# Kernel tuning notes

Hardware: AMD Instinct MI355X
Metric: run time of the kernel (lower is better)

## Reference

```python
import jax, jax.numpy as jnp
import numpy as np

R, A, E, K, NREL = 2048, 16384, 131072, 48, 7
RADIUS = 10.0


def setup_inputs():
    key = jax.random.key(0)
    ks = jax.random.split(key, 20)
    f = jax.random.normal
    return {
        "node_feature": f(ks[0], (R, 21), jnp.float32),
        "all_atom_pos": f(ks[1], (A, 3), jnp.float32) * 8.0,
        "atom_name": jax.random.randint(ks[2], (A,), 0, 38),
        "ca_idx": jax.random.randint(ks[3], (R,), 0, A),
        "edge_src": jax.random.randint(ks[4], (E,), 0, R),
        "edge_dst": jax.random.randint(ks[5], (E,), 0, R),
        "edge_rel": jax.random.randint(ks[6], (E,), 0, NREL),
        # parameters (atom-type embedding table, residue-type linear, AEP point MLP,
        # relational graph conv, env2structures MLP with BN)
        "emb_atom": f(ks[7], (39, 64), jnp.float32) * 0.02,
        "Wres": f(ks[8], (21, 64), jnp.float32) * 0.1,
        "bres": jnp.zeros((64,), jnp.float32),
        "Wxyz": f(ks[9], (3, 64), jnp.float32) * 0.1,
        "W1": f(ks[10], (64, 128), jnp.float32) * 0.1,
        "b1": jnp.zeros((128,), jnp.float32),
        "W2": f(ks[11], (128, 256), jnp.float32) * 0.08,
        "b2": jnp.zeros((256,), jnp.float32),
        "Wconv": f(ks[12], (NREL * 64, 512), jnp.float32) * 0.05,
        "bconv": jnp.zeros((512,), jnp.float32),
        "Wself": f(ks[13], (64, 512), jnp.float32) * 0.1,
        "We1": f(ks[14], (512 + 256, 512), jnp.float32) * 0.05,
        "be1": jnp.zeros((512,), jnp.float32),
        "gamma1": jnp.ones((512,), jnp.float32),
        "beta1": jnp.zeros((512,), jnp.float32),
        "We2": f(ks[15], (512, 512), jnp.float32) * 0.05,
        "be2": jnp.zeros((512,), jnp.float32),
    }


def reference(node_feature, all_atom_pos, atom_name, ca_idx, edge_src, edge_dst, edge_rel,
              emb_atom, Wres, bres, Wxyz, W1, b1, W2, b2,
              Wconv, bconv, Wself, We1, be1, gamma1, beta1, We2, be2):
    # residue-type embedding (nn.Linear(21, 64))
    res_feat = node_feature @ Wres + bres                      # [R,64]
    # ball query: each CA gathers all-atom neighbors within RADIUS (fixed K, masked)
    ca = all_atom_pos[ca_idx]                                   # [R,3]
    diff = ca[:, None, :] - all_atom_pos[None, :, :]            # [R,A,3]
    d = jnp.sqrt(jnp.sum(diff * diff, axis=-1) + 1e-12)         # [R,A]
    dm = jnp.where(d < RADIUS, d, jnp.inf)
    negd, nbr = jax.lax.top_k(-dm, K)                           # K nearest in ball
    mask = (-negd) < RADIUS                                     # [R,K]
    maskf = mask.astype(res_feat.dtype)[..., None]
    delta = (all_atom_pos[nbr] - ca[:, None, :]) * maskf        # relative coords [R,K,3]
    # padded atom-type embedding (padding contributes zeros, like padding_idx=38)
    pts = (emb_atom[atom_name[nbr]] + delta @ Wxyz) * maskf     # [R,K,64]
    # AEP point MLP + masked max-pool -> environment feature
    h = jax.nn.relu(pts @ W1 + b1)                              # [R,K,128]
    env = jnp.max(jnp.where(mask[..., None], h, -1e9), axis=1)  # [R,128]
    env = jax.nn.relu(env @ W2 + b2)                            # [R,256]
    # relational graph conv: per-relation scatter-sum over destination nodes
    seg = edge_dst * NREL + edge_rel
    agg = jax.ops.segment_sum(res_feat[edge_src], seg, num_segments=R * NREL)
    agg = agg.reshape(R, NREL * res_feat.shape[1])              # [R, 7*64]
    hres = jax.nn.relu(agg @ Wconv + bconv + res_feat @ Wself)  # [R,512]
    # env2structures MLP (Linear -> BatchNorm1d(train stats) -> ReLU -> Linear)
    z = jnp.concatenate([hres, env], axis=-1) @ We1 + be1       # [R,512]
    z = (z - z.mean(0)) * jax.lax.rsqrt(z.var(0) + 1e-5) * gamma1 + beta1
    return jax.nn.relu(z) @ We2 + be2                           # [R,512]
```

## Files before the change

### kernel.cpp

```cpp
#include <hip/hip_runtime.h>
#include <math.h>

#define R_ 2048
#define A_ 16384
#define E_ 131072
#define K_ 48
#define NREL_ 7

typedef __attribute__((ext_vector_type(8))) short bfrag8;
typedef __attribute__((ext_vector_type(4))) float f32x4v;

__device__ __forceinline__ unsigned short bf16rne(float f) {
    unsigned u = __builtin_bit_cast(unsigned, f);
    u += 0x7FFFu + ((u >> 16) & 1u);
    return (unsigned short)(u >> 16);
}

__device__ __forceinline__ float dist2(float x, float y, float z,
                                       float cx, float cy, float cz) {
    float dx = x - cx, dy = y - cy, dz = z - cz;
    return fmaf(dx, dx, fmaf(dy, dy, dz * dz));
}

__global__ __launch_bounds__(256) void k_prep(
    const float* __restrict__ Wconv, const float* __restrict__ Wself,
    const float* __restrict__ We1, const float* __restrict__ We2,
    const float* __restrict__ W1,
    const float* __restrict__ node, const float* __restrict__ Wres,
    const float* __restrict__ bres,
    unsigned short* __restrict__ Bt1, unsigned short* __restrict__ Bt2,
    unsigned short* __restrict__ Bt3, unsigned short* __restrict__ W1t,
    float* __restrict__ resfeat, float* __restrict__ bufA,
    float* __restrict__ stats)
{
    int id = blockIdx.x * 256 + threadIdx.x;
    if (id < 262144) {
        int k = id & 511, n = id >> 9;
        float v = (k < 448) ? Wconv[k * 512 + n] : Wself[(k - 448) * 512 + n];
        Bt1[n * 512 + k] = bf16rne(v);
    } else if (id < 655360) {
        int rel = id - 262144;
        int k = rel % 768, n = rel / 768;
        Bt2[n * 768 + k] = bf16rne(We1[k * 512 + n]);
    } else if (id < 917504) {
        int rel = id - 655360;
        int k = rel & 511, n = rel >> 9;
        Bt3[n * 512 + k] = bf16rne(We2[k * 512 + n]);
    } else if (id < 925696) {
        int rel = id - 917504;
        int k = rel & 63, n = rel >> 6;
        W1t[n * 64 + k] = bf16rne(W1[k * 128 + n]);
    } else if (id < 1056768) {
        int rel = id - 925696;
        int r = rel >> 6, c = rel & 63;
        float s = bres[c];
#pragma unroll
        for (int i = 0; i < 21; ++i) s += node[r * 21 + i] * Wres[i * 64 + c];
        resfeat[r * 64 + c] = s;
        bufA[(size_t)r * 512 + 448 + c] = s;
    } else if (id < 1974272) {
        int rel = id - 1056768;
        int r = rel / 448, c = rel % 448;
        bufA[(size_t)r * 512 + c] = 0.f;
    } else if (id < 1975296) {
        stats[id - 1974272] = 0.f;
    }
}

__global__ __launch_bounds__(256) void k_edges(
    const int* __restrict__ esrc, const int* __restrict__ edst,
    const int* __restrict__ erel, const float* __restrict__ resfeat,
    float* __restrict__ bufA)
{
    int idx = blockIdx.x * 256 + threadIdx.x;
    int e = idx >> 6, c = idx & 63;
    int d = edst[e], rel = erel[e], s = esrc[e];
    atomicAdd(&bufA[(size_t)d * 512 + rel * 64 + c], resfeat[s * 64 + c]);
}

__global__ __launch_bounds__(256) void k_ball_env(
    const float* __restrict__ pos, const int* __restrict__ ca_idx,
    const int* __restrict__ atom_name,
    const float* __restrict__ emb, const float* __restrict__ Wxyz,
    const unsigned short* __restrict__ W1t,
    const float* __restrict__ b1,
    const float* __restrict__ W2, const float* __restrict__ b2,
    float* __restrict__ outZ1)
{
    __shared__ __align__(16) char SB[33792];
    __shared__ int s_list[64];
    __shared__ unsigned s_cnt, s_ccnt;
    __shared__ int sB, sNeed, sB2, sNeed2, sTotal;

    unsigned* binsw = (unsigned*)SB;
    unsigned* hist  = (unsigned*)(SB + 16384);
    unsigned* hist2 = (unsigned*)(SB + 17408);
    int*      sc    = (int*)(SB + 18432);
    float*    candd = (float*)(SB + 19456);
    int*      candi = (int*)(SB + 19968);

    float*          pts    = (float*)SB;
    unsigned short* W1s    = (unsigned short*)(SB + 13056);
    float*          sWxyz  = (float*)(SB + 31488);
    float*          s_dv   = (float*)(SB + 32256);
    float*          env128 = (float*)(SB + 32832);
    int*            s_an   = (int*)(SB + 33344);
    int*            s_aa   = (int*)(SB + 33536);

    int tid = threadIdx.x;
    int r = blockIdx.x;
    int ca = ca_idx[r];
    float cx = pos[ca * 3 + 0], cy = pos[ca * 3 + 1], cz = pos[ca * 3 + 2];

    hist[tid] = 0u;
    if (tid == 0) { s_cnt = 0u; s_ccnt = 0u; }
    __syncthreads();

    for (int it = 0; it < 16; ++it) {
        int a0 = it * 1024 + tid * 4;
        const float4* p = (const float4*)(pos + (size_t)a0 * 3);
        float4 p0 = p[0], p1 = p[1], p2 = p[2];
        float xs[4] = { p0.x, p0.w, p1.z, p2.y };
        float ys[4] = { p0.y, p1.x, p1.w, p2.z };
        float zs[4] = { p0.z, p1.y, p2.x, p2.w };
        unsigned pack = 0;
#pragma unroll
        for (int q = 0; q < 4; ++q) {
            float d2 = dist2(xs[q], ys[q], zs[q], cx, cy, cz);
            int b = 255;
            if (d2 < 100.0f) {
                b = (int)(d2 * 2.56f); if (b > 254) b = 254;
                atomicAdd(&hist[b], 1u);
            }
            pack |= (unsigned)b << (q * 8);
        }
        binsw[it * 256 + tid] = pack;
    }
    __syncthreads();

    sc[tid] = (int)hist[tid];
    __syncthreads();
    for (int s = 1; s < 256; s <<= 1) {
        int v = (tid >= s) ? sc[tid - s] : 0;
        __syncthreads();
        sc[tid] += v;
        __syncthreads();
    }
    if (tid == 0) sTotal = sc[255];
    if (sc[tid] >= K_ && (tid == 0 || sc[tid - 1] < K_)) {
        sB = tid;
        sNeed = K_ - (sc[tid] - (int)hist[tid]);
    }
    __syncthreads();

    int mode = (sTotal <= K_) ? 0 : (((int)hist[sB] > 128) ? 2 : 1);

    if (mode <= 1) {
        int B = (mode == 0) ? 255 : sB;
        for (int it = 0; it < 16; ++it) {
            unsigned pack = binsw[it * 256 + tid];
            int a0 = it * 1024 + tid * 4;
#pragma unroll
            for (int q = 0; q < 4; ++q) {
                int b = (pack >> (q * 8)) & 255;
                if (b < B) { unsigned pp = atomicAdd(&s_cnt, 1u); s_list[pp] = a0 + q; }
                else if (b == B && mode == 1) {
                    unsigned c = atomicAdd(&s_ccnt, 1u);
                    if (c < 128u) candi[c] = a0 + q;
                }
            }
        }
    } else {
        int B = sB;
        float lo2 = B * 0.390625f;
        hist2[tid] = 0u;
        __syncthreads();
        for (int it = 0; it < 16; ++it) {
            unsigned pack = binsw[it * 256 + tid];
            int a0 = it * 1024 + tid * 4;
#pragma unroll
            for (int q = 0; q < 4; ++q) {
                if (((pack >> (q * 8)) & 255) == (unsigned)B) {
                    int a = a0 + q;
                    float d2 = dist2(pos[a * 3], pos[a * 3 + 1], pos[a * 3 + 2], cx, cy, cz);
                    int k2 = (int)((d2 - lo2) * 655.36f);
                    if (k2 < 0) k2 = 0; if (k2 > 255) k2 = 255;
                    atomicAdd(&hist2[k2], 1u);
                }
            }
        }
        __syncthreads();
        sc[tid] = (int)hist2[tid];
        __syncthreads();
        for (int s = 1; s < 256; s <<= 1) {
            int v = (tid >= s) ? sc[tid - s] : 0;
            __syncthreads();
            sc[tid] += v;
            __syncthreads();
        }
        if (sc[tid] >= sNeed && (tid == 0 || sc[tid - 1] < sNeed)) {
            sB2 = tid;
            sNeed2 = sNeed - (sc[tid] - (int)hist2[tid]);
        }
        __syncthreads();
        int B2 = sB2;
        for (int it = 0; it < 16; ++it) {
            unsigned pack = binsw[it * 256 + tid];
            int a0 = it * 1024 + tid * 4;
#pragma unroll
            for (int q = 0; q < 4; ++q) {
                int b = (pack >> (q * 8)) & 255;
                if (b < B) { unsigned pp = atomicAdd(&s_cnt, 1u); s_list[pp] = a0 + q; }
                else if (b == B) {
                    int a = a0 + q;
                    float d2 = dist2(pos[a * 3], pos[a * 3 + 1], pos[a * 3 + 2], cx, cy, cz);
                    int k2 = (int)((d2 - lo2) * 655.36f);
                    if (k2 < 0) k2 = 0; if (k2 > 255) k2 = 255;
                    if (k2 < B2) { unsigned pp = atomicAdd(&s_cnt, 1u); s_list[pp] = a; }
                    else if (k2 == B2) {
                        unsigned c = atomicAdd(&s_ccnt, 1u);
                        if (c < 128u) candi[c] = a;
                    }
                }
            }
        }
    }
    __syncthreads();

    int needN = (mode == 0) ? 0 : ((mode == 1) ? sNeed : sNeed2);
    unsigned C = s_ccnt; if (C > 128u) C = 128u;
    if (tid < (int)C) {
        int a = candi[tid];
        float d2 = dist2(pos[a * 3], pos[a * 3 + 1], pos[a * 3 + 2], cx, cy, cz);
        candd[tid] = sqrtf(d2 + 1e-12f);
    }
    __syncthreads();
    if (tid < (int)C) {
        float di = candd[tid]; int ii = candi[tid];
        int rank = 0;
        for (unsigned j = 0; j < C; ++j) {
            float dj = candd[j]; int ij = candi[j];
            if (dj < di || (dj == di && ij < ii)) ++rank;
        }
        if (rank < needN) { unsigned pp = atomicAdd(&s_cnt, 1u); s_list[pp] = ii; }
    }
    __syncthreads();

    unsigned nb = s_cnt;

    for (int c = tid; c < 1024; c += 256)
        *(uint4*)((char*)W1s + (c >> 3) * 144 + (c & 7) * 16) = ((const uint4*)W1t)[c];
    if (tid < 192) sWxyz[tid] = Wxyz[tid];
    if (tid < K_) {
        int a = (tid < (int)nb) ? s_list[tid] : -1;
        s_aa[tid] = a;
        if (a >= 0) {
            s_dv[tid * 3 + 0] = pos[a * 3 + 0] - cx;
            s_dv[tid * 3 + 1] = pos[a * 3 + 1] - cy;
            s_dv[tid * 3 + 2] = pos[a * 3 + 2] - cz;
            s_an[tid] = atom_name[a];
        } else {
            s_dv[tid * 3 + 0] = 0.f; s_dv[tid * 3 + 1] = 0.f; s_dv[tid * 3 + 2] = 0.f;
            s_an[tid] = 0;
        }
    }
    __syncthreads();

    for (int idx = tid; idx < K_ * 64; idx += 256) {
        int row = idx >> 6, k = idx & 63;
        int a = s_aa[row];
        float v = 0.f;
        if (a >= 0) {
            v = emb[s_an[row] * 64 + k]
              + s_dv[row * 3 + 0] * sWxyz[k] + s_dv[row * 3 + 1] * sWxyz[64 + k]
              + s_dv[row * 3 + 2] * sWxyz[128 + k];
        }
        pts[row * 68 + k] = v;
    }
    __syncthreads();

    int w = tid >> 6, l = tid & 63;
    int fr = l & 15, fo = l >> 4;
    f32x4v acc[3][2];
#pragma unroll
    for (int m = 0; m < 3; ++m)
#pragma unroll
        for (int n = 0; n < 2; ++n) acc[m][n] = (f32x4v){0.f, 0.f, 0.f, 0.f};

#pragma unroll
    for (int ks = 0; ks < 2; ++ks) {
        bfrag8 af[3], bf[2];
#pragma unroll
        for (int m = 0; m < 3; ++m) {
            int row = 16 * m + fr;
            const char* base = (const char*)pts + row * 272 + ks * 128 + fo * 32;
            float4 v0 = *(const float4*)base;
            float4 v1 = *(const float4*)(base + 16);
            bfrag8 t;
            t[0] = (short)bf16rne(v0.x); t[1] = (short)bf16rne(v0.y);
            t[2] = (short)bf16rne(v0.z); t[3] = (short)bf16rne(v0.w);
            t[4] = (short)bf16rne(v1.x); t[5] = (short)bf16rne(v1.y);
            t[6] = (short)bf16rne(v1.z); t[7] = (short)bf16rne(v1.w);
            af[m] = t;
        }
#pragma unroll
        for (int n = 0; n < 2; ++n) {
            int wrow = (2 * w + n) * 16 + fr;
            bf[n] = *(const bfrag8*)((const char*)W1s + wrow * 144 + ks * 64 + fo * 16);
        }
#pragma unroll
        for (int m = 0; m < 3; ++m)
#pragma unroll
            for (int n = 0; n < 2; ++n)
                acc[m][n] = __builtin_amdgcn_mfma_f32_16x16x32_bf16(af[m], bf[n], acc[m][n], 0, 0, 0);
    }

#pragma unroll
    for (int n = 0; n < 2; ++n) {
        int col = 32 * w + n * 16 + fr;
        float bv = b1[col];
        float m = -1e30f;
#pragma unroll
        for (int mt = 0; mt < 3; ++mt) {
#pragma unroll
            for (int i = 0; i < 4; ++i) {
                int row = 16 * mt + fo * 4 + i;
                if (s_aa[row] >= 0) m = fmaxf(m, fmaxf(acc[mt][n][i] + bv, 0.f));
            }
        }
        m = fmaxf(m, __shfl_xor(m, 16));
        m = fmaxf(m, __shfl_xor(m, 32));
        if (fo == 0 && (l & 48) == 0) env128[col] = m;
    }
    __syncthreads();

    {
        float s = b2[tid];
        for (int i = 0; i < 128; ++i) s += env128[i] * W2[i * 256 + tid];
        outZ1[(size_t)r * 768 + 512 + tid] = fmaxf(s, 0.f);
    }
}

template<bool RELU_OUT, bool BN_A, bool STATS>
__global__ __launch_bounds__(256) void k_mgemm(
    const float* __restrict__ A, int lda, int K,
    const unsigned short* __restrict__ Bt,
    const float* __restrict__ bias,
    const float* __restrict__ stats, const float* __restrict__ gamma,
    const float* __restrict__ beta,
    float* __restrict__ C, int ldc, float* __restrict__ statsOut)
{
    __shared__ __align__(16) unsigned short As[64 * 32];
    __shared__ __align__(16) unsigned short Bs[64 * 32];
    __shared__ float bnsc[BN_A ? 512 : 1];
    __shared__ float bnsh[BN_A ? 512 : 1];

    int tid = threadIdx.x;
    int m0 = blockIdx.y * 64, n0 = blockIdx.x * 64;

    if (BN_A) {
        for (int i = tid; i < 512; i += 256) {
            float mean = stats[i] * (1.0f / 2048.0f);
            float var = stats[512 + i] * (1.0f / 2048.0f) - mean * mean;
            float inv = 1.0f / sqrtf(var + 1e-5f);
            float scv = gamma[i] * inv;
            bnsc[i] = scv;
            bnsh[i] = beta[i] - mean * scv;
        }
        __syncthreads();
    }

    int w = tid >> 6, l = tid & 63;
    int wm = w >> 1, wn = w & 1;

    int ar = tid >> 2, aslot = tid & 3, acg = aslot * 8;
    int abyte = ar * 64 + ((aslot ^ ((ar >> 1) & 3)) << 4);
    int bn_ = tid >> 2, bslot = tid & 3;
    int bbyte = bn_ * 64 + ((bslot ^ ((bn_ >> 1) & 3)) << 4);

    int fr = l & 15, fo = l >> 4;
    int ar0 = 32 * wm + fr, ar1 = ar0 + 16;
    int af0 = ar0 * 64 + ((fo ^ ((ar0 >> 1) & 3)) << 4);
    int af1 = ar1 * 64 + ((fo ^ ((ar1 >> 1) & 3)) << 4);
    int bc0 = 32 * wn + fr, bc1 = bc0 + 16;
    int bf0o = bc0 * 64 + ((fo ^ ((bc0 >> 1) & 3)) << 4);
    int bf1o = bc1 * 64 + ((fo ^ ((bc1 >> 1) & 3)) << 4);

    f32x4v acc00 = {0.f,0.f,0.f,0.f}, acc01 = {0.f,0.f,0.f,0.f};
    f32x4v acc10 = {0.f,0.f,0.f,0.f}, acc11 = {0.f,0.f,0.f,0.f};

    for (int k0 = 0; k0 < K; k0 += 32) {
        const float* ap = A + (size_t)(m0 + ar) * lda + k0 + acg;
        float4 v0 = *(const float4*)ap;
        float4 v1 = *(const float4*)(ap + 4);
        uint4 bv = *(const uint4*)(Bt + (size_t)(n0 + bn_) * K + k0 + bslot * 8);
        if (BN_A) {
            int kb = k0 + acg;
            v0.x = fmaxf(v0.x * bnsc[kb + 0] + bnsh[kb + 0], 0.f);
            v0.y = fmaxf(v0.y * bnsc[kb + 1] + bnsh[kb + 1], 0.f);
            v0.z = fmaxf(v0.z * bnsc[kb + 2] + bnsh[kb + 2], 0.f);
            v0.w = fmaxf(v0.w * bnsc[kb + 3] + bnsh[kb + 3], 0.f);
            v1.x = fmaxf(v1.x * bnsc[kb + 4] + bnsh[kb + 4], 0.f);
            v1.y = fmaxf(v1.y * bnsc[kb + 5] + bnsh[kb + 5], 0.f);
            v1.z = fmaxf(v1.z * bnsc[kb + 6] + bnsh[kb + 6], 0.f);
            v1.w = fmaxf(v1.w * bnsc[kb + 7] + bnsh[kb + 7], 0.f);
        }
        uint4 aw;
        aw.x = (unsigned)bf16rne(v0.x) | ((unsigned)bf16rne(v0.y) << 16);
        aw.y = (unsigned)bf16rne(v0.z) | ((unsigned)bf16rne(v0.w) << 16);
        aw.z = (unsigned)bf16rne(v1.x) | ((unsigned)bf16rne(v1.y) << 16);
        aw.w = (unsigned)bf16rne(v1.z) | ((unsigned)bf16rne(v1.w) << 16);
        __syncthreads();
        *(uint4*)((char*)As + abyte) = aw;
        *(uint4*)((char*)Bs + bbyte) = bv;
        __syncthreads();

        bfrag8 a0 = *(const bfrag8*)((const char*)As + af0);
        bfrag8 a1 = *(const bfrag8*)((const char*)As + af1);
        bfrag8 b0 = *(const bfrag8*)((const char*)Bs + bf0o);
        bfrag8 b1f = *(const bfrag8*)((const char*)Bs + bf1o);
        acc00 = __builtin_amdgcn_mfma_f32_16x16x32_bf16(a0, b0, acc00, 0, 0, 0);
        acc01 = __builtin_amdgcn_mfma_f32_16x16x32_bf16(a0, b1f, acc01, 0, 0, 0);
        acc10 = __builtin_amdgcn_mfma_f32_16x16x32_bf16(a1, b0, acc10, 0, 0, 0);
        acc11 = __builtin_amdgcn_mfma_f32_16x16x32_bf16(a1, b1f, acc11, 0, 0, 0);
    }

    int col0 = n0 + 32 * wn + fr;
    int row0 = m0 + 32 * wm + fo * 4;
    float bb0 = bias[col0], bb1 = bias[col0 + 16];
    float s0 = 0.f, q0 = 0.f, s1 = 0.f, q1 = 0.f;
#pragma unroll
    for (int i = 0; i < 4; ++i) {
        float u00 = acc00[i] + bb0, u01 = acc01[i] + bb1;
        float u10 = acc10[i] + bb0, u11 = acc11[i] + bb1;
        if (RELU_OUT) {
            u00 = fmaxf(u00, 0.f); u01 = fmaxf(u01, 0.f);
            u10 = fmaxf(u10, 0.f); u11 = fmaxf(u11, 0.f);
        }
        if (STATS) {
            s0 += u00 + u10; q0 += u00 * u00 + u10 * u10;
            s1 += u01 + u11; q1 += u01 * u01 + u11 * u11;
        }
        C[(size_t)(row0 + i) * ldc + col0] = u00;
        C[(size_t)(row0 + i) * ldc + col0 + 16] = u01;
        C[(size_t)(row0 + 16 + i) * ldc + col0] = u10;
        C[(size_t)(row0 + 16 + i) * ldc + col0 + 16] = u11;
    }
    if (STATS) {
        s0 += __shfl_xor(s0, 16); s0 += __shfl_xor(s0, 32);
        q0 += __shfl_xor(q0, 16); q0 += __shfl_xor(q0, 32);
        s1 += __shfl_xor(s1, 16); s1 += __shfl_xor(s1, 32);
        q1 += __shfl_xor(q1, 16); q1 += __shfl_xor(q1, 32);
        if (fo == 0) {
            atomicAdd(&statsOut[col0], s0);
            atomicAdd(&statsOut[512 + col0], q0);
            atomicAdd(&statsOut[col0 + 16], s1);
            atomicAdd(&statsOut[512 + col0 + 16], q1);
        }
    }
}

extern "C" void kernel_launch(void* const* d_in, const int* in_sizes, int n_in,
                              void* d_out, int out_size, void* d_ws, size_t ws_size,
                              hipStream_t stream)
{
    const float* node   = (const float*)d_in[0];
    const float* pos    = (const float*)d_in[1];
    const int*   aname  = (const int*)d_in[2];
    const int*   caidx  = (const int*)d_in[3];
    const int*   esrc   = (const int*)d_in[4];
    const int*   edst   = (const int*)d_in[5];
    const int*   erel   = (const int*)d_in[6];
    const float* emb    = (const float*)d_in[7];
    const float* Wres   = (const float*)d_in[8];
    const float* bres   = (const float*)d_in[9];
    const float* Wxyz   = (const float*)d_in[10];
    const float* W1     = (const float*)d_in[11];
    const float* b1     = (const float*)d_in[12];
    const float* W2     = (const float*)d_in[13];
    const float* b2     = (const float*)d_in[14];
    const float* Wconv  = (const float*)d_in[15];
    const float* bconv  = (const float*)d_in[16];
    const float* Wself  = (const float*)d_in[17];
    const float* We1    = (const float*)d_in[18];
    const float* be1    = (const float*)d_in[19];
    const float* gamma1 = (const float*)d_in[20];
    const float* beta1  = (const float*)d_in[21];
    const float* We2    = (const float*)d_in[22];
    const float* be2    = (const float*)d_in[23];
    float* out = (float*)d_out;

    char* ws = (char*)d_ws;
    float* resfeat = (float*)(ws + 0);
    float* bufA    = (float*)(ws + 524288);
    float* bufZ1   = (float*)(ws + 4718592);
    float* bufZ2   = (float*)(ws + 11010048);
    float* stats   = (float*)(ws + 15204352);
    unsigned short* Bt1 = (unsigned short*)(ws + 15208448);
    unsigned short* Bt2 = (unsigned short*)(ws + 15732736);
    unsigned short* Bt3 = (unsigned short*)(ws + 16519168);
    unsigned short* W1t = (unsigned short*)(ws + 17043456);

    k_prep<<<7716, 256, 0, stream>>>(Wconv, Wself, We1, We2, W1, node, Wres, bres,
                                     Bt1, Bt2, Bt3, W1t, resfeat, bufA, stats);
    k_ball_env<<<R_, 256, 0, stream>>>(pos, caidx, aname, emb, Wxyz, W1t, b1, W2, b2, bufZ1);
    k_edges<<<(size_t)E_ * 64 / 256, 256, 0, stream>>>(esrc, edst, erel, resfeat, bufA);

    dim3 gg(512 / 64, R_ / 64);
    k_mgemm<true, false, false><<<gg, 256, 0, stream>>>(
        bufA, 512, 512, Bt1, bconv, nullptr, nullptr, nullptr, bufZ1, 768, nullptr);
    k_mgemm<false, false, true><<<gg, 256, 0, stream>>>(
        bufZ1, 768, 768, Bt2, be1, nullptr, nullptr, nullptr, bufZ2, 512, stats);
    k_mgemm<false, true, false><<<gg, 256, 0, stream>>>(
        bufZ2, 512, 512, Bt3, be2, stats, gamma1, beta1, out, 512, nullptr);
}
```

Before: 232.0 us.

## Shrink ball-query LDS, read W1 fragments from global, use wave-shuffle scan

Drops the 18 KB LDS staging of W1 and has each wave load its bf16 MFMA B-fragments straight from global/L2. This cuts the block's shared memory from about 34 KB to about 21 KB, and a launch bound of 6 blocks per CU is added to raise occupancy. The two 256-step barrier-heavy histogram prefix scans become a single-wave shuffle scan over 4 bins per lane. The atom-distance loop now processes 8 atoms per thread per iteration with wider loads and packed uint2 stores. The trade-offs are repeated global reads of W1 per block and possible register pressure from the occupancy hint.

Result: faster. 226.7 us (-2.3%).

```diff
diff --git a/kernel.cpp b/kernel.cpp
--- a/kernel.cpp
+++ b/kernel.cpp
@@ -78,7 +78,7 @@
     atomicAdd(&bufA[(size_t)d * 512 + rel * 64 + c], resfeat[s * 64 + c]);
 }
 
-__global__ __launch_bounds__(256) void k_ball_env(
+__global__ __launch_bounds__(256, 6) void k_ball_env(
     const float* __restrict__ pos, const int* __restrict__ ca_idx,
     const int* __restrict__ atom_name,
     const float* __restrict__ emb, const float* __restrict__ Wxyz,
@@ -87,7 +87,7 @@
     const float* __restrict__ W2, const float* __restrict__ b2,
     float* __restrict__ outZ1)
 {
-    __shared__ __align__(16) char SB[33792];
+    __shared__ __align__(16) char SB[20736];
     __shared__ int s_list[64];
     __shared__ unsigned s_cnt, s_ccnt;
     __shared__ int sB, sNeed, sB2, sNeed2, sTotal;
@@ -99,13 +99,12 @@
     float*    candd = (float*)(SB + 19456);
     int*      candi = (int*)(SB + 19968);
 
-    float*          pts    = (float*)SB;
-    unsigned short* W1s    = (unsigned short*)(SB + 13056);
-    float*          sWxyz  = (float*)(SB + 31488);
-    float*          s_dv   = (float*)(SB + 32256);
-    float*          env128 = (float*)(SB + 32832);
-    int*            s_an   = (int*)(SB + 33344);
-    int*            s_aa   = (int*)(SB + 33536);
+    float* pts    = (float*)SB;
+    float* sWxyz  = (float*)(SB + 13056);
+    float* s_dv   = (float*)(SB + 13824);
+    float* env128 = (float*)(SB + 14400);
+    int*   s_an   = (int*)(SB + 14912);
+    int*   s_aa   = (int*)(SB + 15104);
 
     int tid = threadIdx.x;
     int r = blockIdx.x;
@@ -116,36 +115,52 @@
     if (tid == 0) { s_cnt = 0u; s_ccnt = 0u; }
     __syncthreads();
 
-    for (int it = 0; it < 16; ++it) {
-        int a0 = it * 1024 + tid * 4;
+    for (int it = 0; it < 8; ++it) {
+        int a0 = it * 2048 + tid * 8;
         const float4* p = (const float4*)(pos + (size_t)a0 * 3);
-        float4 p0 = p[0], p1 = p[1], p2 = p[2];
-        float xs[4] = { p0.x, p0.w, p1.z, p2.y };
-        float ys[4] = { p0.y, p1.x, p1.w, p2.z };
-        float zs[4] = { p0.z, p1.y, p2.x, p2.w };
-        unsigned pack = 0;
-#pragma unroll
-        for (int q = 0; q < 4; ++q) {
-            float d2 = dist2(xs[q], ys[q], zs[q], cx, cy, cz);
-            int b = 255;
-            if (d2 < 100.0f) {
-                b = (int)(d2 * 2.56f); if (b > 254) b = 254;
-                atomicAdd(&hist[b], 1u);
+        float4 pv[6];
+#pragma unroll
+        for (int j = 0; j < 6; ++j) pv[j] = p[j];
+        unsigned pk[2] = { 0u, 0u };
+#pragma unroll
+        for (int g = 0; g < 2; ++g) {
+            float4 p0 = pv[g * 3], p1 = pv[g * 3 + 1], p2 = pv[g * 3 + 2];
+            float xs[4] = { p0.x, p0.w, p1.z, p2.y };
+            float ys[4] = { p0.y, p1.x, p1.w, p2.z };
+            float zs[4] = { p0.z, p1.y, p2.x, p2.w };
+#pragma unroll
+            for (int q = 0; q < 4; ++q) {
+                float d2 = dist2(xs[q], ys[q], zs[q], cx, cy, cz);
+                int b = 255;
+                if (d2 < 100.0f) {
+                    b = (int)(d2 * 2.56f); if (b > 254) b = 254;
+                    atomicAdd(&hist[b], 1u);
+                }
+                pk[g] |= (unsigned)b << (q * 8);
             }
-            pack |= (unsigned)b << (q * 8);
-        }
-        binsw[it * 256 + tid] = pack;
-    }
-    __syncthreads();
-
-    sc[tid] = (int)hist[tid];
-    __syncthreads();
-    for (int s = 1; s < 256; s <<= 1) {
-        int v = (tid >= s) ? sc[tid - s] : 0;
-        __syncthreads();
-        sc[tid] += v;
-        __syncthreads();
-    }
+        }
+        *(uint2*)&binsw[it * 512 + tid * 2] = make_uint2(pk[0], pk[1]);
+    }
+    __syncthreads();
+
+    if (tid < 64) {
+        int base = tid * 4;
+        int v0 = (int)hist[base], v1 = (int)hist[base + 1];
+        int v2 = (int)hist[base + 2], v3 = (int)hist[base + 3];
+        int loc1 = v0, loc2 = v0 + v1, loc3 = v0 + v1 + v2;
+        int s = loc3 + v3;
+        int inc = s;
+        for (int off = 1; off < 64; off <<= 1) {
+            int u = __shfl_up(inc, off);
+            if (tid >= off) inc += u;
+        }
+        int excl = inc - s;
+        sc[base] = excl + v0;
+        sc[base + 1] = excl + loc1 + v1;
+        sc[base + 2] = excl + loc2 + v2;
+        sc[base + 3] = excl + loc3 + v3;
+    }
+    __syncthreads();
     if (tid == 0) sTotal = sc[255];
     if (sc[tid] >= K_ && (tid == 0 || sc[tid - 1] < K_)) {
         sB = tid;
@@ -157,16 +172,21 @@
 
     if (mode <= 1) {
         int B = (mode == 0) ? 255 : sB;
-        for (int it = 0; it < 16; ++it) {
-            unsigned pack = binsw[it * 256 + tid];
-            int a0 = it * 1024 + tid * 4;
-#pragma unroll
-            for (int q = 0; q < 4; ++q) {
-                int b = (pack >> (q * 8)) & 255;
-                if (b < B) { unsigned pp = atomicAdd(&s_cnt, 1u); s_list[pp] = a0 + q; }
-                else if (b == B && mode == 1) {
-                    unsigned c = atomicAdd(&s_ccnt, 1u);
-                    if (c < 128u) candi[c] = a0 + q;
+        for (int it = 0; it < 8; ++it) {
+            uint2 pks = *(const uint2*)&binsw[it * 512 + tid * 2];
+            unsigned pkz[2] = { pks.x, pks.y };
+            int abase = it * 2048 + tid * 8;
+#pragma unroll
+            for (int g = 0; g < 2; ++g) {
+                int a0 = abase + g * 4;
+#pragma unroll
+                for (int q = 0; q < 4; ++q) {
+                    int b = (pkz[g] >> (q * 8)) & 255;
+                    if (b < B) { unsigned pp = atomicAdd(&s_cnt, 1u); s_list[pp] = a0 + q; }
+                    else if (b == B && mode == 1) {
+                        unsigned c = atomicAdd(&s_ccnt, 1u);
+                        if (c < 128u) candi[c] = a0 + q;
+                    }
                 }
             }
         }
@@ -175,51 +195,69 @@
         float lo2 = B * 0.390625f;
         hist2[tid] = 0u;
         __syncthreads();
-        for (int it = 0; it < 16; ++it) {
-            unsigned pack = binsw[it * 256 + tid];
-            int a0 = it * 1024 + tid * 4;
-#pragma unroll
-            for (int q = 0; q < 4; ++q) {
-                if (((pack >> (q * 8)) & 255) == (unsigned)B) {
-                    int a = a0 + q;
-                    float d2 = dist2(pos[a * 3], pos[a * 3 + 1], pos[a * 3 + 2], cx, cy, cz);
-                    int k2 = (int)((d2 - lo2) * 655.36f);
-                    if (k2 < 0) k2 = 0; if (k2 > 255) k2 = 255;
-                    atomicAdd(&hist2[k2], 1u);
+        for (int it = 0; it < 8; ++it) {
+            uint2 pks = *(const uint2*)&binsw[it * 512 + tid * 2];
+            unsigned pkz[2] = { pks.x, pks.y };
+            int abase = it * 2048 + tid * 8;
+#pragma unroll
+            for (int g = 0; g < 2; ++g) {
+#pragma unroll
+                for (int q = 0; q < 4; ++q) {
+                    if (((pkz[g] >> (q * 8)) & 255) == (unsigned)B) {
+                        int a = abase + g * 4 + q;
+                        float d2 = dist2(pos[a * 3], pos[a * 3 + 1], pos[a * 3 + 2], cx, cy, cz);
+                        int k2 = (int)((d2 - lo2) * 655.36f);
+                        if (k2 < 0) k2 = 0; if (k2 > 255) k2 = 255;
+                        atomicAdd(&hist2[k2], 1u);
+                    }
                 }
             }
         }
         __syncthreads();
-        sc[tid] = (int)hist2[tid];
-        __syncthreads();
-        for (int s = 1; s < 256; s <<= 1) {
-            int v = (tid >= s) ? sc[tid - s] : 0;
-            __syncthreads();
-            sc[tid] += v;
-            __syncthreads();
-        }
+        if (tid < 64) {
+            int base = tid * 4;
+            int v0 = (int)hist2[base], v1 = (int)hist2[base + 1];
+            int v2 = (int)hist2[base + 2], v3 = (int)hist2[base + 3];
+            int loc1 = v0, loc2 = v0 + v1, loc3 = v0 + v1 + v2;
+            int s = loc3 + v3;
+            int inc = s;
+            for (int off = 1; off < 64; off <<= 1) {
+                int u = __shfl_up(inc, off);
+                if (tid >= off) inc += u;
+            }
+            int excl = inc - s;
+            sc[base] = excl + v0;
+            sc[base + 1] = excl + loc1 + v1;
+            sc[base + 2] = excl + loc2 + v2;
+            sc[base + 3] = excl + loc3 + v3;
+        }
+        __syncthreads();
         if (sc[tid] >= sNeed && (tid == 0 || sc[tid - 1] < sNeed)) {
             sB2 = tid;
             sNeed2 = sNeed - (sc[tid] - (int)hist2[tid]);
         }
         __syncthreads();
         int B2 = sB2;
-        for (int it = 0; it < 16; ++it) {
-            unsigned pack = binsw[it * 256 + tid];
-            int a0 = it * 1024 + tid * 4;
-#pragma unroll
-            for (int q = 0; q < 4; ++q) {
-                int b = (pack >> (q * 8)) & 255;
-                if (b < B) { unsigned pp = atomicAdd(&s_cnt, 1u); s_list[pp] = a0 + q; }
-                else if (b == B) {
-                    int a = a0 + q;
-                    float d2 = dist2(pos[a * 3], pos[a * 3 + 1], pos[a * 3 + 2], cx, cy, cz);
-                    int k2 = (int)((d2 - lo2) * 655.36f);
-                    if (k2 < 0) k2 = 0; if (k2 > 255) k2 = 255;
-                    if (k2 < B2) { unsigned pp = atomicAdd(&s_cnt, 1u); s_list[pp] = a; }
-                    else if (k2 == B2) {
-                        unsigned c = atomicAdd(&s_ccnt, 1u);
-                        if (c < 128u) candi[c] = a;
+        for (int it = 0; it < 8; ++it) {
+            uint2 pks = *(const uint2*)&binsw[it * 512 + tid * 2];
+            unsigned pkz[2] = { pks.x, pks.y };
+            int abase = it * 2048 + tid * 8;
+#pragma unroll
+            for (int g = 0; g < 2; ++g) {
+#pragma unroll
+                for (int q = 0; q < 4; ++q) {
+                    int b = (pkz[g] >> (q * 8)) & 255;
+                    int a = abase + g * 4 + q;
+                    if (b < B) { unsigned pp = atomicAdd(&s_cnt, 1u); s_list[pp] = a; }
+                    else if (b == B) {
+                        float d2 = dist2(pos[a * 3], pos[a * 3 + 1], pos[a * 3 + 2], cx, cy, cz);
+                        int k2 = (int)((d2 - lo2) * 655.36f);
+                        if (k2 < 0) k2 = 0; if (k2 > 255) k2 = 255;
+                        if (k2 < B2) { unsigned pp = atomicAdd(&s_cnt, 1u); s_list[pp] = a; }
+                        else if (k2 == B2) {
+                            unsigned c = atomicAdd(&s_ccnt, 1u);
+                            if (c < 128u) candi[c] = a;
+                        }
                     }
                 }
             }
@@ -247,9 +285,6 @@
     __syncthreads();
 
     unsigned nb = s_cnt;
-
-    for (int c = tid; c < 1024; c += 256)
-        *(uint4*)((char*)W1s + (c >> 3) * 144 + (c & 7) * 16) = ((const uint4*)W1t)[c];
     if (tid < 192) sWxyz[tid] = Wxyz[tid];
     if (tid < K_) {
         int a = (tid < (int)nb) ? s_list[tid] : -1;
@@ -291,6 +326,11 @@
     for (int ks = 0; ks < 2; ++ks) {
         bfrag8 af[3], bf[2];
 #pragma unroll
+        for (int n = 0; n < 2; ++n) {
+            int wrow = (2 * w + n) * 16 + fr;
+            bf[n] = *(const bfrag8*)((const char*)W1t + wrow * 128 + ks * 64 + fo * 16);
+        }
+#pragma unroll
         for (int m = 0; m < 3; ++m) {
             int row = 16 * m + fr;
             const char* base = (const char*)pts + row * 272 + ks * 128 + fo * 32;
@@ -302,11 +342,6 @@
             t[4] = (short)bf16rne(v1.x); t[5] = (short)bf16rne(v1.y);
             t[6] = (short)bf16rne(v1.z); t[7] = (short)bf16rne(v1.w);
             af[m] = t;
-        }
-#pragma unroll
-        for (int n = 0; n < 2; ++n) {
-            int wrow = (2 * w + n) * 16 + fr;
-            bf[n] = *(const bfrag8*)((const char*)W1s + wrow * 144 + ks * 64 + fo * 16);
         }
 #pragma unroll
         for (int m = 0; m < 3; ++m)
```
